# Performance work log

Measured on AMD Instinct MI355X. Metric: run time of the kernel, lower is better.

Reference implementation:

```python
import jax, jax.numpy as jnp
import numpy as np

B, T, DV, H, DW, V, MAXLEN = 64, 32, 2048, 1024, 512, 20000, 3


def setup_inputs() -> dict:
    key = jax.random.key(0)
    ks = jax.random.split(key, 14)
    s = 1.0 / np.sqrt(H)

    def rn(k, shape, scale):
        return jax.random.normal(k, shape, jnp.float32) * scale

    return {
        "vid_feats": jax.random.normal(ks[0], (B, T, DV), jnp.float32),
        "W_ih1": rn(ks[1], (3 * H, DV), s),
        "W_hh1": rn(ks[2], (3 * H, H), s),
        "b_ih1": rn(ks[3], (3 * H,), s),
        "b_hh1": rn(ks[4], (3 * H,), s),
        "W_ih2": rn(ks[5], (3 * H, H + DW), s),
        "W_hh2": rn(ks[6], (3 * H, H), s),
        "b_ih2": rn(ks[7], (3 * H,), s),
        "b_hh2": rn(ks[8], (3 * H,), s),
        "W_obj": rn(ks[9], (V, H), s),
        "b_obj": rn(ks[10], (V,), s),
        "W_rel": rn(ks[11], (V, H), s),
        "b_rel": rn(ks[12], (V,), s),
    }


def _gru_cell(x_proj, h, W_hh, b_hh):
    # PyTorch GRU gate math. x_proj = x @ W_ih.T + b_ih (precomputed).
    hp = h @ W_hh.T + b_hh
    xr, xz, xn = jnp.split(x_proj, 3, axis=-1)
    hr, hz, hn = jnp.split(hp, 3, axis=-1)
    r = jax.nn.sigmoid(xr + hr)
    z = jax.nn.sigmoid(xz + hz)
    n = jnp.tanh(xn + r * hn)
    return (1.0 - z) * n + z * h


def reference(vid_feats, W_ih1, W_hh1, b_ih1, b_hh1,
              W_ih2, W_hh2, b_ih2, b_hh2,
              W_obj, b_obj, W_rel, b_rel):
    Bsz = vid_feats.shape[0]
    Hh = W_hh1.shape[1]
    dtype = vid_feats.dtype

    # ---- encoder: rnn1 over video frames (input projection batched) ----
    xp1 = jnp.einsum('btd,gd->btg', vid_feats, W_ih1) + b_ih1  # [B,T,3H]

    def step1(h, xp):
        h = _gru_cell(xp, h, W_hh1, b_hh1)
        return h, h

    h1, out1 = jax.lax.scan(step1, jnp.zeros((Bsz, Hh), dtype),
                            jnp.swapaxes(xp1, 0, 1))  # out1: [T,B,H]

    # ---- rnn2 over concat(out1, zero word embeddings): zero part drops out ----
    W_ih2_h = W_ih2[:, :Hh]  # columns multiplying the hidden part
    xp2 = jnp.einsum('tbh,gh->tbg', out1, W_ih2_h) + b_ih2  # [T,B,3H]

    def step2(h, xp):
        return _gru_cell(xp, h, W_hh2, b_hh2), None

    h2, _ = jax.lax.scan(step2, jnp.zeros((Bsz, Hh), dtype), xp2)

    # ---- decode loop: zero frame / zero word inputs each step ----
    xp1_pad = jnp.broadcast_to(b_ih1, (Bsz, b_ih1.shape[0]))
    probs = []
    for i in range(MAXLEN):
        h1 = _gru_cell(xp1_pad, h1, W_hh1, b_hh1)
        xp2_t = h1 @ W_ih2_h.T + b_ih2
        h2 = _gru_cell(xp2_t, h2, W_hh2, b_hh2)
        if i != 1:
            logits = h2 @ W_obj.T + b_obj
        else:
            logits = h2 @ W_rel.T + b_rel
        probs.append(jax.nn.log_softmax(logits, axis=-1))
    return jnp.stack(probs, axis=1)  # [B, MAXLEN, V]
```

## Files before the change

### kernel.cpp

```cpp
#include <hip/hip_runtime.h>
#include <math.h>

#define Bsz 64
#define Tt  32
#define TTOT 35
#define Dv  2048
#define Hd  1024
#define G3  3072
#define Vv  20000
#define ML  3
#define NTILE 1250
#define FSTR 16

typedef __attribute__((ext_vector_type(8))) short bf16x8;
typedef __attribute__((ext_vector_type(4))) float f32x4;
typedef unsigned long long u64;
#define MFMA(a,b,c) __builtin_amdgcn_mfma_f32_16x16x32_bf16(a,b,c,0,0,0)

__device__ __forceinline__ short f2bf(float f) {
    union { float f; unsigned u; } v; v.f = f;
    unsigned r = v.u + 0x7fffu + ((v.u >> 16) & 1u);
    return (short)(r >> 16);
}
__device__ __forceinline__ void cvt8(const float* __restrict__ s,
                                     short* __restrict__ d) {
    float4 x = *(const float4*)s;
    float4 y = *(const float4*)(s + 4);
    bf16x8 o;
    o[0]=f2bf(x.x); o[1]=f2bf(x.y); o[2]=f2bf(x.z); o[3]=f2bf(x.w);
    o[4]=f2bf(y.x); o[5]=f2bf(y.y); o[6]=f2bf(y.z); o[7]=f2bf(y.w);
    *(bf16x8*)d = o;
}
__device__ __forceinline__ bf16x8 pack8(const float* __restrict__ s) {
    float4 x = *(const float4*)s;
    float4 y = *(const float4*)(s + 4);
    bf16x8 o;
    o[0]=f2bf(x.x); o[1]=f2bf(x.y); o[2]=f2bf(x.z); o[3]=f2bf(x.w);
    o[4]=f2bf(y.x); o[5]=f2bf(y.y); o[6]=f2bf(y.z); o[7]=f2bf(y.w);
    return o;
}
__device__ __forceinline__ bf16x8 pack2(const float4& x, const float4& y) {
    bf16x8 o;
    o[0]=f2bf(x.x); o[1]=f2bf(x.y); o[2]=f2bf(x.z); o[3]=f2bf(x.w);
    o[4]=f2bf(y.x); o[5]=f2bf(y.y); o[6]=f2bf(y.z); o[7]=f2bf(y.w);
    return o;
}

__device__ __forceinline__ void poll_flags(const unsigned* fl, unsigned tgt) {
    const int lane = threadIdx.x & 63;
    const unsigned* p = &fl[lane * FSTR];
    unsigned f = __hip_atomic_load(p, __ATOMIC_RELAXED, __HIP_MEMORY_SCOPE_AGENT);
    while (!__all((int)(f >= tgt))) {
        __builtin_amdgcn_s_sleep(2);
        f = __hip_atomic_load(p, __ATOMIC_RELAXED, __HIP_MEMORY_SCOPE_AGENT);
    }
}

__global__ __launch_bounds__(256)
void cvt2(const float* __restrict__ vid,  short* __restrict__ vid_bf,
          const float* __restrict__ Wih1, short* __restrict__ Wih1_bf)
{
    const long b0 = 524288;
    const long b1 = b0 + 786432;
    for (long i = (long)blockIdx.x * 256 + threadIdx.x; i < b1;
         i += (long)gridDim.x * 256) {
        if (i < b0) cvt8(vid + i * 8, vid_bf + i * 8);
        else { const long q = i - b0; cvt8(Wih1 + q * 8, Wih1_bf + q * 8); }
    }
}

__global__ __launch_bounds__(256)
void gemm_xp1(const short* __restrict__ vid_bf,
              const short* __restrict__ Wih1_bf,
              const float* __restrict__ b_ih1,
              float* __restrict__ xp1)
{
    __shared__ __align__(16) short As[8 * 64 * 8];
    __shared__ __align__(16) short Bs[8 * 64 * 8];
    const int tid = threadIdx.x;
    const int w = tid >> 6, l = tid & 63;
    const int wm = w >> 1, wn = w & 1;
    const int lr = l & 15, lg = l >> 4;
    const int m0 = blockIdx.y * 128, n0 = blockIdx.x * 128;

    f32x4 acc[4][4] = {};

    for (int k0 = 0; k0 < Dv; k0 += 32) {
        #pragma unroll
        for (int i = 0; i < 2; ++i) {
            const int q  = i * 256 + tid;
            const int r  = ((q >> 6) << 4) | (q & 15);
            const int sc = (q >> 4) & 3;
            const int m  = m0 + r;
            const int arow = (m & 63) * Tt + (m >> 6);
            __builtin_amdgcn_global_load_lds(
                (const void*)(vid_bf + (size_t)arow * Dv + k0 + sc * 8),
                (void*)(As + q * 8), 16, 0, 0);
            __builtin_amdgcn_global_load_lds(
                (const void*)(Wih1_bf + (size_t)(n0 + r) * Dv + k0 + sc * 8),
                (void*)(Bs + q * 8), 16, 0, 0);
        }
        __syncthreads();
        bf16x8 af[4], bfr[4];
        #pragma unroll
        for (int mt = 0; mt < 4; ++mt) {
            af[mt]  = *(const bf16x8*)(As + ((wm * 4 + mt) * 64 + l) * 8);
            bfr[mt] = *(const bf16x8*)(Bs + ((wn * 4 + mt) * 64 + l) * 8);
        }
        #pragma unroll
        for (int mt = 0; mt < 4; ++mt)
            #pragma unroll
            for (int nt = 0; nt < 4; ++nt)
                acc[mt][nt] = MFMA(af[mt], bfr[nt], acc[mt][nt]);
        __syncthreads();
    }

    #pragma unroll
    for (int mt = 0; mt < 4; ++mt)
        #pragma unroll
        for (int nt = 0; nt < 4; ++nt)
            #pragma unroll
            for (int v = 0; v < 4; ++v) {
                const int m = m0 + wm * 64 + mt * 16 + lg * 4 + v;
                const int n = n0 + wn * 64 + nt * 16 + lr;
                xp1[(size_t)m * G3 + n] = acc[mt][nt][v] + b_ih1[n];
            }
}

__global__ __launch_bounds__(256, 1)
void mega(const float* __restrict__ xp1, const float* __restrict__ b_ih1,
          const float* __restrict__ Whh1f, const float* __restrict__ b_hh1,
          const float* __restrict__ Wih2f, const float* __restrict__ b_ih2,
          const float* __restrict__ Whh2f, const float* __restrict__ b_hh2,
          short* __restrict__ out1h,
          float* __restrict__ xp2s,
          short* __restrict__ h2h,
          unsigned* __restrict__ flags1, unsigned* __restrict__ flagsP,
          unsigned* __restrict__ flags2)
{
    __shared__ __align__(16) short Wl[4 * 3 * 8 * 64 * 8];
    __shared__ __align__(16) float xch[4][4][3][256];
    __shared__ __align__(16) short hstage[64][16];
    const int tid = threadIdx.x;
    const int w  = tid >> 6;
    const int l  = tid & 63;
    const int lr = l & 15, lg = l >> 4;
    const int role = blockIdx.x >> 6;
    const int k    = blockIdx.x & 63;
    const int j0 = k * 16;
    const int j  = j0 + lr;

    const float* Wf = (role == 0) ? Whh1f : (role == 1) ? Wih2f : Whh2f;
    const int ldw   = (role == 1) ? (Hd + 512) : Hd;
    const float* bias = (role == 0) ? b_hh1 : (role == 1) ? b_ih2 : b_hh2;

    #pragma unroll
    for (int g = 0; g < 3; ++g)
        #pragma unroll
        for (int ks = 0; ks < 8; ++ks) {
            const float* src = Wf + (size_t)(g * Hd + j) * ldw + w * 256 + ks * 32 + lg * 8;
            *(bf16x8*)(Wl + ((((w * 3 + g) * 8 + ks) * 64) + l) * 8) = pack8(src);
        }

    const float b0 = bias[j], b1 = bias[Hd + j], b2 = bias[2 * Hd + j];
    short* Ab = (role == 2) ? h2h : out1h;

    float bxr = 0.f, bxz = 0.f, bxn = 0.f;
    float hp[4] = {0.f, 0.f, 0.f, 0.f};
    float xr[4], xz[4], xn[4];
    if (role == 0) {
        bxr = b_ih1[j]; bxz = b_ih1[Hd + j]; bxn = b_ih1[2 * Hd + j];
        #pragma unroll
        for (int v = 0; v < 4; ++v) {
            const int b = w * 16 + lg * 4 + v;
            const float* xrow = xp1 + (size_t)b * G3;
            xr[v] = xrow[j]; xz[v] = xrow[Hd + j]; xn[v] = xrow[2 * Hd + j];
        }
    }
    __syncthreads();

    for (int t = 0; t < TTOT; ++t) {
        if (role == 0)      { if (w == 0) poll_flags(flags1, (unsigned)t); }
        else if (role == 1) { if (w == 0) poll_flags(flags1, (unsigned)(t + 1)); }
        else {
            if (w == 0)      poll_flags(flagsP, (unsigned)(t + 1));
            else if (w == 1) poll_flags(flags2, (unsigned)t);
        }
        __syncthreads();
        asm volatile("" ::: "memory");

        const short* hin = Ab + (size_t)(role == 1 ? t + 1 : t) * (64 * Hd);
        bf16x8 A[4][8];
        #pragma unroll
        for (int mt = 0; mt < 4; ++mt)
            #pragma unroll
            for (int ks = 0; ks < 8; ++ks)
                A[mt][ks] = *(const bf16x8*)(hin + (size_t)(mt * 16 + lr) * Hd
                                             + w * 256 + ks * 32 + lg * 8);
        if (role == 2) {
            #pragma unroll
            for (int v = 0; v < 4; ++v) {
                const int b = w * 16 + lg * 4 + v;
                const float* xrow = xp2s + ((size_t)t * 64 + b) * G3;
                xr[v] = xrow[j]; xz[v] = xrow[Hd + j]; xn[v] = xrow[2 * Hd + j];
            }
        }

        f32x4 acc[4][3] = {};
        #pragma unroll
        for (int ks = 0; ks < 8; ++ks) {
            bf16x8 B0 = *(const bf16x8*)(Wl + ((((w * 3 + 0) * 8 + ks) * 64) + l) * 8);
            bf16x8 B1 = *(const bf16x8*)(Wl + ((((w * 3 + 1) * 8 + ks) * 64) + l) * 8);
            bf16x8 B2 = *(const bf16x8*)(Wl + ((((w * 3 + 2) * 8 + ks) * 64) + l) * 8);
            #pragma unroll
            for (int mt = 0; mt < 4; ++mt) {
                acc[mt][0] = MFMA(A[mt][ks], B0, acc[mt][0]);
                acc[mt][1] = MFMA(A[mt][ks], B1, acc[mt][1]);
                acc[mt][2] = MFMA(A[mt][ks], B2, acc[mt][2]);
            }
        }

        #pragma unroll
        for (int mt = 0; mt < 4; ++mt)
            #pragma unroll
            for (int g = 0; g < 3; ++g)
                *(f32x4*)&xch[w][mt][g][l * 4] = acc[mt][g];
        __syncthreads();
        f32x4 tot[3];
        #pragma unroll
        for (int g = 0; g < 3; ++g) {
            f32x4 t0 = *(const f32x4*)&xch[0][w][g][l * 4];
            f32x4 t1 = *(const f32x4*)&xch[1][w][g][l * 4];
            f32x4 t2 = *(const f32x4*)&xch[2][w][g][l * 4];
            f32x4 t3 = *(const f32x4*)&xch[3][w][g][l * 4];
            tot[g] = (t0 + t1) + (t2 + t3);
        }

        if (role == 1) {
            const float bg[3] = {b0, b1, b2};
            #pragma unroll
            for (int v = 0; v < 4; ++v) {
                const int b = w * 16 + lg * 4 + v;
                #pragma unroll
                for (int g = 0; g < 3; ++g) {
                    union { float f; unsigned u; } cv;
                    cv.f = tot[g][v] + bg[g];
                    __hip_atomic_store(
                        (unsigned*)(xp2s + ((size_t)t * 64 + b) * G3 + g * Hd + j),
                        cv.u, __ATOMIC_RELAXED, __HIP_MEMORY_SCOPE_AGENT);
                }
            }
            __syncthreads();
        } else {
            #pragma unroll
            for (int v = 0; v < 4; ++v) {
                const int b = w * 16 + lg * 4 + v;
                const float rg = 1.f / (1.f + __expf(-(xr[v] + tot[0][v] + b0)));
                const float zg = 1.f / (1.f + __expf(-(xz[v] + tot[1][v] + b1)));
                const float ng = tanhf(xn[v] + rg * (tot[2][v] + b2));
                const float hv = (1.f - zg) * ng + zg * hp[v];
                hp[v] = hv;
                hstage[b][lr] = f2bf(hv);
            }
            if (role == 0) {
                if (t + 1 < Tt) {
                    #pragma unroll
                    for (int v = 0; v < 4; ++v) {
                        const int b = w * 16 + lg * 4 + v;
                        const float* xrow = xp1 + (size_t)((t + 1) * 64 + b) * G3;
                        xr[v] = xrow[j]; xz[v] = xrow[Hd + j]; xn[v] = xrow[2 * Hd + j];
                    }
                } else {
                    #pragma unroll
                    for (int v = 0; v < 4; ++v) { xr[v]=bxr; xz[v]=bxz; xn[v]=bxn; }
                }
            }
            __syncthreads();
            {
                const int b = tid >> 2, part = tid & 3;
                const u64 pv = *(const u64*)&hstage[b][part * 4];
                __hip_atomic_store(
                    (u64*)(Ab + (size_t)(t + 1) * (64 * Hd) + b * Hd + j0 + part * 4),
                    pv, __ATOMIC_RELAXED, __HIP_MEMORY_SCOPE_AGENT);
            }
            __syncthreads();
        }

        if (tid == 0) {
            unsigned* fl = (role == 0) ? flags1 : (role == 1) ? flagsP : flags2;
            __hip_atomic_store(&fl[k * FSTR], (unsigned)(t + 1),
                               __ATOMIC_RELAXED, __HIP_MEMORY_SCOPE_AGENT);
        }
    }
}

__global__ __launch_bounds__(256)
void logits_dual(const short* __restrict__ h2h,
                 const float* __restrict__ Wobj, const float* __restrict__ bobj,
                 const float* __restrict__ Wrel, const float* __restrict__ brel,
                 float* __restrict__ logits3)
{
    const int tid = threadIdx.x;
    const int w = tid >> 6, l = tid & 63;
    const int lr = l & 15, lg = l >> 4;
    const bool dual = blockIdx.x < 313;
    const int nb = dual ? blockIdx.x : blockIdx.x - 313;
    const int tile = nb * 4 + w;
    if (tile >= NTILE) return;
    const int n0 = tile * 16;
    const float* Wo = dual ? Wobj : Wrel;
    const float* bo = dual ? bobj : brel;
    const short* h0 = dual ? (h2h + (size_t)33 * 64 * Hd)
                           : (h2h + (size_t)34 * 64 * Hd);
    const short* hC = h2h + (size_t)35 * 64 * Hd;

    const float* wbase = Wo + (size_t)(n0 + lr) * Hd + lg * 8;
    const short* abase = h0 + (size_t)lr * Hd + lg * 8;
    const short* cbase = hC + (size_t)lr * Hd + lg * 8;

    f32x4 accA[4] = {}, accC[4] = {};

    float4 wx[8], wy[8];
    #pragma unroll
    for (int i = 0; i < 8; ++i) {
        wx[i] = *(const float4*)(wbase + i * 32);
        wy[i] = *(const float4*)(wbase + i * 32 + 4);
    }

    #pragma unroll
    for (int kc = 0; kc < 8; ++kc) {
        bf16x8 Ach[4][4], Cch[4][4];
        #pragma unroll
        for (int u = 0; u < 4; ++u) {
            const int ks = kc * 4 + u;
            #pragma unroll
            for (int mt = 0; mt < 4; ++mt)
                Ach[mt][u] = *(const bf16x8*)(abase + (size_t)(mt * 16) * Hd + ks * 32);
        }
        if (dual) {
            #pragma unroll
            for (int u = 0; u < 4; ++u) {
                const int ks = kc * 4 + u;
                #pragma unroll
                for (int mt = 0; mt < 4; ++mt)
                    Cch[mt][u] = *(const bf16x8*)(cbase + (size_t)(mt * 16) * Hd + ks * 32);
            }
        }
        #pragma unroll
        for (int u = 0; u < 4; ++u) {
            const int ks = kc * 4 + u;
            const int bi = ks & 7;
            const bf16x8 wv = pack2(wx[bi], wy[bi]);
            if (ks < 24) {
                wx[bi] = *(const float4*)(wbase + (ks + 8) * 32);
                wy[bi] = *(const float4*)(wbase + (ks + 8) * 32 + 4);
            }
            #pragma unroll
            for (int mt = 0; mt < 4; ++mt) {
                accA[mt] = MFMA(Ach[mt][u], wv, accA[mt]);
                if (dual) accC[mt] = MFMA(Cch[mt][u], wv, accC[mt]);
            }
        }
    }

    const float bn = bo[n0 + lr];
    float* lg0 = logits3 + (size_t)(dual ? 0 : 1) * 64 * Vv;
    float* lg2 = logits3 + (size_t)2 * 64 * Vv;
    #pragma unroll
    for (int mt = 0; mt < 4; ++mt)
        #pragma unroll
        for (int v = 0; v < 4; ++v) {
            const size_t row = (size_t)(mt * 16 + lg * 4 + v) * Vv + n0 + lr;
            lg0[row] = accA[mt][v] + bn;
            if (dual) lg2[row] = accC[mt][v] + bn;
        }
}

__global__ __launch_bounds__(256)
void log_softmax_all(const float* __restrict__ logits3, float* __restrict__ out)
{
    __shared__ float red[4];
    const int step = blockIdx.x >> 6;
    const int b    = blockIdx.x & 63;
    const int tid  = threadIdx.x;
    const float* row = logits3 + ((size_t)step * 64 + b) * Vv;

    float m = -1e30f;
    for (int v = tid; v < Vv; v += 256) m = fmaxf(m, row[v]);
    #pragma unroll
    for (int off = 32; off > 0; off >>= 1) m = fmaxf(m, __shfl_down(m, off, 64));
    if ((tid & 63) == 0) red[tid >> 6] = m;
    __syncthreads();
    m = fmaxf(fmaxf(red[0], red[1]), fmaxf(red[2], red[3]));
    __syncthreads();

    float s = 0.f;
    for (int v = tid; v < Vv; v += 256) s += expf(row[v] - m);
    #pragma unroll
    for (int off = 32; off > 0; off >>= 1) s += __shfl_down(s, off, 64);
    if ((tid & 63) == 0) red[tid >> 6] = s;
    __syncthreads();
    s = red[0] + red[1] + red[2] + red[3];
    const float lse = m + logf(s);

    float* orow = out + ((size_t)b * ML + step) * Vv;
    for (int v = tid; v < Vv; v += 256) orow[v] = row[v] - lse;
}

extern "C" void kernel_launch(void* const* d_in, const int* in_sizes, int n_in,
                              void* d_out, int out_size, void* d_ws, size_t ws_size,
                              hipStream_t stream)
{
    (void)in_sizes; (void)n_in; (void)out_size; (void)ws_size;
    const float* vid   = (const float*)d_in[0];
    const float* W_ih1 = (const float*)d_in[1];
    const float* W_hh1 = (const float*)d_in[2];
    const float* b_ih1 = (const float*)d_in[3];
    const float* b_hh1 = (const float*)d_in[4];
    const float* W_ih2 = (const float*)d_in[5];
    const float* W_hh2 = (const float*)d_in[6];
    const float* b_ih2 = (const float*)d_in[7];
    const float* b_hh2 = (const float*)d_in[8];
    const float* W_obj = (const float*)d_in[9];
    const float* b_obj = (const float*)d_in[10];
    const float* W_rel = (const float*)d_in[11];
    const float* b_rel = (const float*)d_in[12];
    float* out = (float*)d_out;

    char* p = (char*)d_ws;
    short* vid_bf   = (short*)p; p += (size_t)2048 * Dv * 2;
    short* Wih1_bf  = (short*)p; p += (size_t)G3 * Dv * 2;
    unsigned int* flg = (unsigned int*)p; p += 16384;
    short* out1h  = (short*)p; p += (size_t)36 * 64 * Hd * 2;
    short* h2h    = (short*)p; p += (size_t)36 * 64 * Hd * 2;
    float* xp1    = (float*)p; p += (size_t)2048 * G3 * 4;
    float* xp2s   = (float*)p; p += (size_t)TTOT * 64 * G3 * 4;
    float* logits3= (float*)p; p += (size_t)ML * 64 * Vv * 4;

    unsigned* flags1 = flg;
    unsigned* flagsP = flg + 1024;
    unsigned* flags2 = flg + 2048;

    hipMemsetAsync(flg, 0, 16384, stream);
    hipMemsetAsync(out1h, 0, (size_t)64 * Hd * 2, stream);
    hipMemsetAsync(h2h,   0, (size_t)64 * Hd * 2, stream);

    cvt2<<<1280, 256, 0, stream>>>(vid, vid_bf, W_ih1, Wih1_bf);

    gemm_xp1<<<dim3(G3 / 128, 2048 / 128), 256, 0, stream>>>(
        vid_bf, Wih1_bf, b_ih1, xp1);

    mega<<<192, 256, 0, stream>>>(
        xp1, b_ih1, W_hh1, b_hh1, W_ih2, b_ih2, W_hh2, b_hh2,
        out1h, xp2s, h2h, flags1, flagsP, flags2);

    logits_dual<<<626, 256, 0, stream>>>(h2h, W_obj, b_obj, W_rel, b_rel, logits3);

    log_softmax_all<<<192, 256, 0, stream>>>(logits3, out);
}
```

Before: 462.9 us.

## Convert output projection weights to bf16 alongside xp1 GEMM to halve logits traffic

Adds 320 extra blocks to the xp1 GEMM launch that convert W_obj and W_rel from fp32 to bf16 in workspace, using a 1D grid remap. The logits kernel gets a bf16-weight variant that loads bf16x8 directly, halving its weight bytes and dropping the pack step. The conversion itself still reads 160MB and writes 80MB every call, so it only pays off if it overlaps with or is cheaper than the fp32 reads it replaces. A fallback to the fp32 path is kept when the workspace is too small.

```diff
diff --git a/kernel.cpp b/kernel.cpp
--- a/kernel.cpp
+++ b/kernel.cpp
@@ -73,15 +73,31 @@
 void gemm_xp1(const short* __restrict__ vid_bf,
               const short* __restrict__ Wih1_bf,
               const float* __restrict__ b_ih1,
-              float* __restrict__ xp1)
+              float* __restrict__ xp1,
+              const float* __restrict__ Wobj, const float* __restrict__ Wrel,
+              short* __restrict__ Wobj_bf, short* __restrict__ Wrel_bf,
+              int do_cvt)
 {
     __shared__ __align__(16) short As[8 * 64 * 8];
     __shared__ __align__(16) short Bs[8 * 64 * 8];
     const int tid = threadIdx.x;
+
+    if (blockIdx.x >= 384) {
+        if (do_cvt) {
+            const int cb = blockIdx.x - 384;
+            const long NC = (long)Vv * Hd / 8;
+            for (long i = (long)cb * 256 + tid; i < 2 * NC; i += 320L * 256) {
+                if (i < NC) cvt8(Wobj + i * 8, Wobj_bf + i * 8);
+                else { const long q = i - NC; cvt8(Wrel + q * 8, Wrel_bf + q * 8); }
+            }
+        }
+        return;
+    }
+
     const int w = tid >> 6, l = tid & 63;
     const int wm = w >> 1, wn = w & 1;
     const int lr = l & 15, lg = l >> 4;
-    const int m0 = blockIdx.y * 128, n0 = blockIdx.x * 128;
+    const int m0 = (blockIdx.x / 24) * 128, n0 = (blockIdx.x % 24) * 128;
 
     f32x4 acc[4][4] = {};
 
@@ -294,10 +310,11 @@
     }
 }
 
+template<bool WBF16>
 __global__ __launch_bounds__(256)
 void logits_dual(const short* __restrict__ h2h,
-                 const float* __restrict__ Wobj, const float* __restrict__ bobj,
-                 const float* __restrict__ Wrel, const float* __restrict__ brel,
+                 const void* __restrict__ Wobj, const float* __restrict__ bobj,
+                 const void* __restrict__ Wrel, const float* __restrict__ brel,
                  float* __restrict__ logits3)
 {
     const int tid = threadIdx.x;
@@ -308,57 +325,95 @@
     const int tile = nb * 4 + w;
     if (tile >= NTILE) return;
     const int n0 = tile * 16;
-    const float* Wo = dual ? Wobj : Wrel;
+    const void* Wo = dual ? Wobj : Wrel;
     const float* bo = dual ? bobj : brel;
     const short* h0 = dual ? (h2h + (size_t)33 * 64 * Hd)
                            : (h2h + (size_t)34 * 64 * Hd);
     const short* hC = h2h + (size_t)35 * 64 * Hd;
-
-    const float* wbase = Wo + (size_t)(n0 + lr) * Hd + lg * 8;
     const short* abase = h0 + (size_t)lr * Hd + lg * 8;
     const short* cbase = hC + (size_t)lr * Hd + lg * 8;
 
     f32x4 accA[4] = {}, accC[4] = {};
 
-    float4 wx[8], wy[8];
-    #pragma unroll
-    for (int i = 0; i < 8; ++i) {
-        wx[i] = *(const float4*)(wbase + i * 32);
-        wy[i] = *(const float4*)(wbase + i * 32 + 4);
-    }
-
-    #pragma unroll
-    for (int kc = 0; kc < 8; ++kc) {
-        bf16x8 Ach[4][4], Cch[4][4];
-        #pragma unroll
-        for (int u = 0; u < 4; ++u) {
-            const int ks = kc * 4 + u;
-            #pragma unroll
-            for (int mt = 0; mt < 4; ++mt)
-                Ach[mt][u] = *(const bf16x8*)(abase + (size_t)(mt * 16) * Hd + ks * 32);
-        }
-        if (dual) {
+    if constexpr (WBF16) {
+        const short* wbase = (const short*)Wo + (size_t)(n0 + lr) * Hd + lg * 8;
+        bf16x8 wr[4];
+        #pragma unroll
+        for (int i = 0; i < 4; ++i) wr[i] = *(const bf16x8*)(wbase + i * 32);
+
+        #pragma unroll
+        for (int kc = 0; kc < 16; ++kc) {
+            bf16x8 Ach[4][2], Cch[4][2];
+            #pragma unroll
+            for (int u = 0; u < 2; ++u) {
+                const int ks = kc * 2 + u;
+                #pragma unroll
+                for (int mt = 0; mt < 4; ++mt)
+                    Ach[mt][u] = *(const bf16x8*)(abase + (size_t)(mt * 16) * Hd + ks * 32);
+            }
+            if (dual) {
+                #pragma unroll
+                for (int u = 0; u < 2; ++u) {
+                    const int ks = kc * 2 + u;
+                    #pragma unroll
+                    for (int mt = 0; mt < 4; ++mt)
+                        Cch[mt][u] = *(const bf16x8*)(cbase + (size_t)(mt * 16) * Hd + ks * 32);
+                }
+            }
+            #pragma unroll
+            for (int u = 0; u < 2; ++u) {
+                const int ks = kc * 2 + u;
+                const int bi = ks & 3;
+                const bf16x8 wv = wr[bi];
+                if (ks < 28) wr[bi] = *(const bf16x8*)(wbase + (ks + 4) * 32);
+                #pragma unroll
+                for (int mt = 0; mt < 4; ++mt) {
+                    accA[mt] = MFMA(Ach[mt][u], wv, accA[mt]);
+                    if (dual) accC[mt] = MFMA(Cch[mt][u], wv, accC[mt]);
+                }
+            }
+        }
+    } else {
+        const float* wbase = (const float*)Wo + (size_t)(n0 + lr) * Hd + lg * 8;
+        float4 wx[8], wy[8];
+        #pragma unroll
+        for (int i = 0; i < 8; ++i) {
+            wx[i] = *(const float4*)(wbase + i * 32);
+            wy[i] = *(const float4*)(wbase + i * 32 + 4);
+        }
+        #pragma unroll
+        for (int kc = 0; kc < 8; ++kc) {
+            bf16x8 Ach[4][4], Cch[4][4];
             #pragma unroll
             for (int u = 0; u < 4; ++u) {
                 const int ks = kc * 4 + u;
                 #pragma unroll
                 for (int mt = 0; mt < 4; ++mt)
-                    Cch[mt][u] = *(const bf16x8*)(cbase + (size_t)(mt * 16) * Hd + ks * 32);
-            }
-        }
-        #pragma unroll
-        for (int u = 0; u < 4; ++u) {
-            const int ks = kc * 4 + u;
-            const int bi = ks & 7;
-            const bf16x8 wv = pack2(wx[bi], wy[bi]);
-            if (ks < 24) {
-                wx[bi] = *(const float4*)(wbase + (ks + 8) * 32);
-                wy[bi] = *(const float4*)(wbase + (ks + 8) * 32 + 4);
-            }
-            #pragma unroll
-            for (int mt = 0; mt < 4; ++mt) {
-                accA[mt] = MFMA(Ach[mt][u], wv, accA[mt]);
-                if (dual) accC[mt] = MFMA(Cch[mt][u], wv, accC[mt]);
+                    Ach[mt][u] = *(const bf16x8*)(abase + (size_t)(mt * 16) * Hd + ks * 32);
+            }
+            if (dual) {
+                #pragma unroll
+                for (int u = 0; u < 4; ++u) {
+                    const int ks = kc * 4 + u;
+                    #pragma unroll
+                    for (int mt = 0; mt < 4; ++mt)
+                        Cch[mt][u] = *(const bf16x8*)(cbase + (size_t)(mt * 16) * Hd + ks * 32);
+                }
+            }
+            #pragma unroll
+            for (int u = 0; u < 4; ++u) {
+                const int ks = kc * 4 + u;
+                const int bi = ks & 7;
+                const bf16x8 wv = pack2(wx[bi], wy[bi]);
+                if (ks < 24) {
+                    wx[bi] = *(const float4*)(wbase + (ks + 8) * 32);
+                    wy[bi] = *(const float4*)(wbase + (ks + 8) * 32 + 4);
+                }
+                #pragma unroll
+                for (int mt = 0; mt < 4; ++mt) {
+                    accA[mt] = MFMA(Ach[mt][u], wv, accA[mt]);
+                    if (dual) accC[mt] = MFMA(Cch[mt][u], wv, accC[mt]);
+                }
             }
         }
     }
@@ -411,7 +466,7 @@
                               void* d_out, int out_size, void* d_ws, size_t ws_size,
                               hipStream_t stream)
 {
-    (void)in_sizes; (void)n_in; (void)out_size; (void)ws_size;
+    (void)in_sizes; (void)n_in; (void)out_size;
     const float* vid   = (const float*)d_in[0];
     const float* W_ih1 = (const float*)d_in[1];
     const float* W_hh1 = (const float*)d_in[2];
@@ -436,6 +491,9 @@
     float* xp1    = (float*)p; p += (size_t)2048 * G3 * 4;
     float* xp2s   = (float*)p; p += (size_t)TTOT * 64 * G3 * 4;
     float* logits3= (float*)p; p += (size_t)ML * 64 * Vv * 4;
+    short* Wobj_bf = (short*)p; p += (size_t)Vv * Hd * 2;
+    short* Wrel_bf = (short*)p; p += (size_t)Vv * Hd * 2;
+    const int use_bf = ((size_t)(p - (char*)d_ws) <= ws_size) ? 1 : 0;
 
     unsigned* flags1 = flg;
     unsigned* flagsP = flg + 1024;
@@ -447,14 +505,19 @@
 
     cvt2<<<1280, 256, 0, stream>>>(vid, vid_bf, W_ih1, Wih1_bf);
 
-    gemm_xp1<<<dim3(G3 / 128, 2048 / 128), 256, 0, stream>>>(
-        vid_bf, Wih1_bf, b_ih1, xp1);
+    gemm_xp1<<<704, 256, 0, stream>>>(vid_bf, Wih1_bf, b_ih1, xp1,
+                                      W_obj, W_rel, Wobj_bf, Wrel_bf, use_bf);
 
     mega<<<192, 256, 0, stream>>>(
         xp1, b_ih1, W_hh1, b_hh1, W_ih2, b_ih2, W_hh2, b_hh2,
         out1h, xp2s, h2h, flags1, flagsP, flags2);
 
-    logits_dual<<<626, 256, 0, stream>>>(h2h, W_obj, b_obj, W_rel, b_rel, logits3);
+    if (use_bf)
+        logits_dual<true><<<626, 256, 0, stream>>>(
+            h2h, (const void*)Wobj_bf, b_obj, (const void*)Wrel_bf, b_rel, logits3);
+    else
+        logits_dual<false><<<626, 256, 0, stream>>>(
+            h2h, (const void*)W_obj, b_obj, (const void*)W_rel, b_rel, logits3);
 
     log_softmax_all<<<192, 256, 0, stream>>>(logits3, out);
 }
```

Result: slower. 488.7 us (+5.6%).
